# Kernel optimization log

Measured on AMD Instinct MI355X. Metric: run time of the kernel, lower is better.

The kernel has to match this reference:

```python
import jax, jax.numpy as jnp
import numpy as np

D_MODEL = 1024
NUM_HEADS = 16
HEAD_DIM = D_MODEL // NUM_HEADS
B, L = 4, 2048


def setup_inputs() -> dict:
    key = jax.random.key(0)
    ks = jax.random.split(key, 10)
    s = 1.0 / np.sqrt(D_MODEL)
    inp = {
        "x": jax.random.normal(ks[0], (B, L, D_MODEL), dtype=jnp.float32),
        "mask": jax.random.randint(ks[1], (1, 1, L, L), 0, 2, dtype=jnp.int32),
        "Wq": jax.random.normal(ks[2], (D_MODEL, D_MODEL), dtype=jnp.float32) * s,
        "bq": jnp.zeros((D_MODEL,), dtype=jnp.float32),
        "Wk": jax.random.normal(ks[3], (D_MODEL, D_MODEL), dtype=jnp.float32) * s,
        "bk": jnp.zeros((D_MODEL,), dtype=jnp.float32),
        "Wv": jax.random.normal(ks[4], (D_MODEL, D_MODEL), dtype=jnp.float32) * s,
        "bv": jnp.zeros((D_MODEL,), dtype=jnp.float32),
        "Wo": jax.random.normal(ks[5], (D_MODEL, D_MODEL), dtype=jnp.float32) * s,
        "bo": jnp.zeros((D_MODEL,), dtype=jnp.float32),
    }
    return inp


def reference(x, mask, Wq, bq, Wk, bk, Wv, bv, Wo, bo):
    b, l, d = x.shape
    # projections (torch Linear: x @ W.T + b)
    q = (x @ Wq.T + bq).reshape(b, l, NUM_HEADS, HEAD_DIM).transpose(0, 2, 1, 3)
    k = (x @ Wk.T + bk).reshape(b, l, NUM_HEADS, HEAD_DIM).transpose(0, 2, 1, 3)
    v = (x @ Wv.T + bv).reshape(b, l, NUM_HEADS, HEAD_DIM).transpose(0, 2, 1, 3)
    scale = 1.0 / np.sqrt(HEAD_DIM).astype(np.float32)
    scores = jnp.einsum("bhqd,bhkd->bhqk", q, k) * scale
    scores = jnp.where(mask == 0, jnp.float32(-1e9), scores)
    attn = jax.nn.softmax(scores, axis=-1)
    out = jnp.einsum("bhqk,bhkd->bhqd", attn, v)
    out = out.transpose(0, 2, 1, 3).reshape(b, l, d)
    return out @ Wo.T + bo
```

## Files before the change

### kernel.cpp

```cpp
#include <hip/hip_runtime.h>
#include <stdint.h>

#define LSEQ 2048
#define DMODEL 1024
#define NHEADS 16
#define HDIM 64
#define NBATCH 4

typedef __attribute__((ext_vector_type(8))) __bf16 bf16x8;
typedef __attribute__((ext_vector_type(4))) __bf16 bf16x4;
typedef __attribute__((ext_vector_type(4))) float f32x4;
typedef __attribute__((ext_vector_type(16))) float f32x16;
typedef __attribute__((ext_vector_type(4))) uint32_t u32x4;
typedef __attribute__((ext_vector_type(8))) uint16_t u16x8;

__device__ inline float fexp2(float x) {
#if __has_builtin(__builtin_amdgcn_exp2f)
    return __builtin_amdgcn_exp2f(x);
#else
    float r; asm("v_exp_f32 %0, %1" : "=v"(r) : "v"(x)); return r;
#endif
}

__device__ inline uint32_t bitmask1(uint32_t m, int pos) {
#if __has_builtin(__builtin_amdgcn_sbfe)
    return (uint32_t)__builtin_amdgcn_sbfe((int)m, pos, 1);
#else
    return (uint32_t)(((int32_t)(m << (31 - pos))) >> 31);
#endif
}

__device__ inline uint32_t cvtpk(float lo, float hi) {
    uint32_t r;
    asm("v_cvt_pk_bf16_f32 %0, %1, %2" : "=v"(r) : "v"(lo), "v"(hi));
    return r;
}
__device__ inline void swap32(uint32_t& a, uint32_t& b) {
    asm volatile("v_permlane32_swap_b32 %0, %1" : "+v"(a), "+v"(b));
}

__device__ inline void gload_lds16(const void* g, const void* l) {
    auto gp = reinterpret_cast<const uint32_t __attribute__((address_space(1)))*>(
        reinterpret_cast<uintptr_t>(g));
    auto lp = reinterpret_cast<uint32_t __attribute__((address_space(3)))*>(
        (uint32_t)(uintptr_t)(l));
    __builtin_amdgcn_global_load_lds(gp, lp, 16, 0, 0);
}

__device__ inline f32x16 zero16() {
    f32x16 z;
#pragma unroll
    for (int i = 0; i < 16; i++) z[i] = 0.f;
    return z;
}

__global__ void cvt_f32_bf16(const float* __restrict__ src, __bf16* __restrict__ dst, int n) {
    int idx = blockIdx.x * blockDim.x + threadIdx.x;
    int stride = gridDim.x * blockDim.x;
    for (int i = idx * 4; i < n; i += stride * 4) {
        float4 f = *(const float4*)(src + i);
        bf16x4 v;
        v[0] = (__bf16)f.x; v[1] = (__bf16)f.y; v[2] = (__bf16)f.z; v[3] = (__bf16)f.w;
        *(bf16x4*)(dst + i) = v;
    }
}

__global__ void cvt_w4(const float* __restrict__ a, const float* __restrict__ b,
                       const float* __restrict__ c, const float* __restrict__ d,
                       __bf16* __restrict__ dst) {
    const int t = blockIdx.x * blockDim.x + threadIdx.x;
    const int i4 = t * 4;
    const int m = i4 >> 20;
    const int off = i4 & ((1 << 20) - 1);
    const float* src = (m == 0) ? a : (m == 1) ? b : (m == 2) ? c : d;
    float4 f = *(const float4*)(src + off);
    bf16x4 v;
    v[0] = (__bf16)f.x; v[1] = (__bf16)f.y; v[2] = (__bf16)f.z; v[3] = (__bf16)f.w;
    *(bf16x4*)(dst + i4) = v;
}

__global__ void pack_bias(const float* __restrict__ bq, const float* __restrict__ bk,
                          const float* __restrict__ bv, float* __restrict__ dst) {
    const int i = blockIdx.x * 256 + threadIdx.x;
    dst[i] = (i < 1024) ? bq[i] : (i < 2048) ? bk[i - 1024] : bv[i - 2048];
}

__global__ void pack_mask(const int* __restrict__ mask, unsigned long long* __restrict__ mbits) {
    const int row = blockIdx.x;
    const int w = threadIdx.x >> 6, lane = threadIdx.x & 63;
    const int* mrow = mask + (size_t)row * LSEQ;
#pragma unroll
    for (int it = 0; it < 8; it++) {
        const int c = it * 256 + w * 64 + lane;
        const unsigned long long b = __ballot(mrow[c] != 0);
        if (lane == 0) mbits[(size_t)row * 32 + it * 4 + w] = b;
    }
}

template <int MODE>
__global__ __launch_bounds__(256) void gemm_bt(const __bf16* __restrict__ A,
                                               const __bf16* __restrict__ Bw,
                                               const float* __restrict__ bias,
                                               void* __restrict__ Cout,
                                               int M, int N, int K, float scale) {
    __shared__ __bf16 As[128 * 32];
    __shared__ __bf16 Bs[128 * 32];

    const int nwg = gridDim.x;
    int bid = blockIdx.x;
    bid = (bid & 7) * (nwg >> 3) + (bid >> 3);

    const int nbn = N >> 7;
    const int bm = (bid / nbn) << 7;
    const int bn = (bid % nbn) << 7;
    const int tid = threadIdx.x;
    const int w = tid >> 6, lane = tid & 63;
    const int l15 = lane & 15, l4 = lane >> 4;
    const int wm = (w >> 1) * 64, wn = (w & 1) * 64;

    f32x4 acc[4][4];
    for (int i = 0; i < 4; i++)
        for (int j = 0; j < 4; j++)
            acc[i][j] = (f32x4){0.f, 0.f, 0.f, 0.f};

    const int fa0 = (w * 2 + 0) * 64 + lane;
    const int fa1 = (w * 2 + 1) * 64 + lane;
    const __bf16* gA0 = A + (size_t)(bm + (fa0 >> 2)) * K + (fa0 & 3) * 8;
    const __bf16* gA1 = A + (size_t)(bm + (fa1 >> 2)) * K + (fa1 & 3) * 8;
    const __bf16* gB0 = Bw + (size_t)(bn + (fa0 >> 2)) * K + (fa0 & 3) * 8;
    const __bf16* gB1 = Bw + (size_t)(bn + (fa1 >> 2)) * K + (fa1 & 3) * 8;
    const __bf16* lA0 = &As[(w * 2 + 0) * 512];
    const __bf16* lA1 = &As[(w * 2 + 1) * 512];
    const __bf16* lB0 = &Bs[(w * 2 + 0) * 512];
    const __bf16* lB1 = &Bs[(w * 2 + 1) * 512];

    for (int kt = 0; kt < K; kt += 32) {
        __syncthreads();
        gload_lds16(gA0 + kt, lA0);
        gload_lds16(gA1 + kt, lA1);
        gload_lds16(gB0 + kt, lB0);
        gload_lds16(gB1 + kt, lB1);
        __syncthreads();

        bf16x8 af[4], bw[4];
        for (int i = 0; i < 4; i++)
            af[i] = *(const bf16x8*)&As[(wm + i * 16 + l15) * 32 + l4 * 8];
        for (int j = 0; j < 4; j++)
            bw[j] = *(const bf16x8*)&Bs[(wn + j * 16 + l15) * 32 + l4 * 8];
        for (int i = 0; i < 4; i++)
            for (int j = 0; j < 4; j++)
                acc[i][j] = __builtin_amdgcn_mfma_f32_16x16x32_bf16(af[i], bw[j], acc[i][j], 0, 0, 0);
    }

    for (int i = 0; i < 4; i++) {
        const int row0 = bm + wm + i * 16 + l4 * 4;
        for (int j = 0; j < 4; j++) {
            const int col = bn + wn + j * 16 + l15;
            const float bv = bias[col];
            if (MODE == 0) {
                __bf16* dst = (__bf16*)Cout;
                const int which = col >> 10;
                const int cr = col & 1023;
                const int h = cr >> 6, d = cr & 63;
                const float scl = (which == 0) ? scale : 1.0f;
                for (int jj = 0; jj < 4; jj++) {
                    const int r = row0 + jj;
                    const int b = r >> 11, l = r & (LSEQ - 1);
                    dst[((size_t)which << 23) +
                        (((size_t)(b * NHEADS + h) * LSEQ + l) << 6) + d] =
                        (__bf16)((acc[i][j][jj] + bv) * scl);
                }
            } else {
                float* dst = (float*)Cout;
                for (int jj = 0; jj < 4; jj++) {
                    const int r = row0 + jj;
                    dst[(size_t)r * N + col] = acc[i][j][jj] + bv;
                }
            }
        }
    }
}

__device__ inline void storeV8(uint32_t (*vt)[32], int kpi, int d0,
                               const u16x8& r0, const u16x8& r1) {
    const uint32_t* a = (const uint32_t*)&r0;
    const uint32_t* b = (const uint32_t*)&r1;
#pragma unroll
    for (int jp = 0; jp < 4; jp++) {
        const uint32_t w0 = __builtin_amdgcn_perm(b[jp], a[jp], 0x05040100u);
        const uint32_t w1 = __builtin_amdgcn_perm(b[jp], a[jp], 0x07060302u);
        const int j0 = jp * 2, j1 = jp * 2 + 1;
        vt[d0 + j0][(kpi & 3) | (((kpi >> 2) ^ j0) << 2)] = w0;
        vt[d0 + j1][(kpi & 3) | (((kpi >> 2) ^ j1) << 2)] = w1;
    }
}

__global__ __launch_bounds__(256) void attn_fwd(const __bf16* __restrict__ Q,
                                                const __bf16* __restrict__ Kk,
                                                const __bf16* __restrict__ V,
                                                const unsigned long long* __restrict__ mbits,
                                                __bf16* __restrict__ Oout) {
    const int bh = blockIdx.x & 63;
    const int qt = blockIdx.x >> 6;
    const int tid = threadIdx.x;
    const int w = tid >> 6, lane = tid & 63;
    const int l31 = lane & 31, hi = lane >> 5, l7 = lane & 7;

    __shared__ __bf16 Ks[2][64 * 64];
    __shared__ uint32_t Vt32[2][64][32];

    const int q0w = qt * 128 + w * 32;

    const __bf16* qrow = Q + ((size_t)bh * LSEQ + q0w + l31) * HDIM + hi * 8;
    bf16x8 aq[4];
#pragma unroll
    for (int s = 0; s < 4; s++) aq[s] = *(const bf16x8*)(qrow + s * 16);

    f32x16 o0 = zero16(), o1 = zero16();
    float m_run = -1.0e30f, l_run = 0.f;

    const int ck0 = tid, ck1 = tid + 256;
    const int koff0 = ((ck0 >> 3) << 7) + ((((ck0 & 7) ^ ((ck0 >> 3) & 7))) << 4);
    const int koff1 = ((ck1 >> 3) << 7) + ((((ck1 & 7) ^ ((ck1 >> 3) & 7))) << 4);
    const char* kp0 = (const char*)(Kk + (size_t)bh * LSEQ * HDIM) + koff0;
    const char* kp1 = (const char*)(Kk + (size_t)bh * LSEQ * HDIM) + koff1;

    const int kpi = tid & 31;
    const int d0v = (tid >> 5) * 8;
    const __bf16* vp0 = V + (size_t)bh * LSEQ * HDIM + (size_t)(2 * kpi) * HDIM + d0v;
    const __bf16* vp1 = vp0 + HDIM;

    const uint2* mptr = (const uint2*)(mbits + (size_t)(q0w + l31) * 32);
    const int msh = hi * 4;

    {
        const u16x8 v0 = *(const u16x8*)(vp0);
        const u16x8 v1 = *(const u16x8*)(vp1);
        vp0 += 64 * HDIM; vp1 += 64 * HDIM;
        storeV8(Vt32[0], kpi, d0v, v0, v1);
        gload_lds16(kp0, &Ks[0][ck0 * 8]);
        gload_lds16(kp1, &Ks[0][ck1 * 8]);
        kp0 += 8192; kp1 += 8192;
    }
    __syncthreads();

    int cur = 0;
    const int NT = LSEQ / 64;
    for (int t = 0; t < NT; t++) {
        const int nx = cur ^ 1;
        u16x8 nv0, nv1;
        if (t < NT - 1) {
            nv0 = *(const u16x8*)(vp0);
            nv1 = *(const u16x8*)(vp1);
            vp0 += 64 * HDIM; vp1 += 64 * HDIM;
            gload_lds16(kp0, &Ks[nx][ck0 * 8]);
            gload_lds16(kp1, &Ks[nx][ck1 * 8]);
            kp0 += 8192; kp1 += 8192;
        }

        const uint2 mw = mptr[t];
        const uint32_t mword0 = mw.x >> msh;
        const uint32_t mword1 = mw.y >> msh;
        const char* ksb = (const char*)&Ks[cur][0];
        const uint32_t* vb = &Vt32[cur][0][0];

#pragma unroll
        for (int kk = 0; kk < 2; kk++) {
            f32x16 sf = zero16();
            __builtin_amdgcn_s_setprio(1);
#pragma unroll
            for (int s = 0; s < 4; s++) {
                const bf16x8 ka = *(const bf16x8*)(ksb + kk * 4096 + l31 * 128 +
                                                   (((s * 2 + hi) ^ l7) << 4));
                sf = __builtin_amdgcn_mfma_f32_32x32x16_bf16(ka, aq[s], sf, 0, 0, 0);
            }
            __builtin_amdgcn_s_setprio(0);

            float vmx = sf[0];
#pragma unroll
            for (int r = 1; r < 16; r++) vmx = fmaxf(vmx, sf[r]);
            vmx = fmaxf(vmx, __shfl_xor(vmx, 32));

            if (__any(vmx > m_run + 8.f)) {
                const float mnew = fmaxf(m_run, vmx);
                const float alpha = fexp2(m_run - mnew);
                m_run = mnew;
                l_run *= alpha;
#pragma unroll
                for (int r = 0; r < 16; r++) {
                    const float ar = __shfl(alpha, (r & 3) + 8 * (r >> 2) + 4 * hi);
                    o0[r] *= ar; o1[r] *= ar;
                }
            }

            const uint32_t mwd = kk ? mword1 : mword0;
            float e[16];
#pragma unroll
            for (int r = 0; r < 16; r++) {
                float ev = fexp2(sf[r] - m_run);
                const uint32_t msk = bitmask1(mwd, (r & 3) + 8 * (r >> 2));
                ev = __builtin_bit_cast(float, __builtin_bit_cast(uint32_t, ev) & msk);
                l_run += ev;
                e[r] = ev;
            }
            uint32_t p0 = cvtpk(e[0], e[1]),   p1 = cvtpk(e[2], e[3]);
            uint32_t p2 = cvtpk(e[4], e[5]),   p3 = cvtpk(e[6], e[7]);
            uint32_t p4 = cvtpk(e[8], e[9]),   p5 = cvtpk(e[10], e[11]);
            uint32_t p6 = cvtpk(e[12], e[13]), p7 = cvtpk(e[14], e[15]);
            swap32(p0, p2); swap32(p1, p3);
            swap32(p4, p6); swap32(p5, p7);
            const bf16x8 pa0 = __builtin_bit_cast(bf16x8, (u32x4){p0, p1, p2, p3});
            const bf16x8 pa1 = __builtin_bit_cast(bf16x8, (u32x4){p4, p5, p6, p7});

            __builtin_amdgcn_s_setprio(1);
#pragma unroll
            for (int s2 = 0; s2 < 2; s2++) {
                const bf16x8 pa = s2 ? pa1 : pa0;
                const int col = (((kk * 4 + s2 * 2 + hi) ^ l7) << 2);
                const u32x4 v0 = *(const u32x4*)(vb + (l31) * 32 + col);
                const u32x4 v1 = *(const u32x4*)(vb + (32 + l31) * 32 + col);
                o0 = __builtin_amdgcn_mfma_f32_32x32x16_bf16(pa, __builtin_bit_cast(bf16x8, v0), o0, 0, 0, 0);
                o1 = __builtin_amdgcn_mfma_f32_32x32x16_bf16(pa, __builtin_bit_cast(bf16x8, v1), o1, 0, 0, 0);
            }
            __builtin_amdgcn_s_setprio(0);
        }

        if (t < NT - 1) storeV8(Vt32[nx], kpi, d0v, nv0, nv1);
        __syncthreads();
        cur = nx;
    }

    const int b = bh >> 4, h = bh & 15;
    const float lt = l_run + __shfl_xor(l_run, 32);
    const float inv = 1.0f / fmaxf(lt, 1e-30f);
#pragma unroll
    for (int r = 0; r < 16; r++) {
        const int ql = (r & 3) + 8 * (r >> 2) + 4 * hi;
        const float invr = __shfl(inv, ql);
        const int q = q0w + ql;
        const size_t base = ((size_t)b * LSEQ + q) * DMODEL + h * HDIM + l31;
        Oout[base] = (__bf16)(o0[r] * invr);
        Oout[base + 32] = (__bf16)(o1[r] * invr);
    }
}

extern "C" void kernel_launch(void* const* d_in, const int* in_sizes, int n_in,
                              void* d_out, int out_size, void* d_ws, size_t ws_size,
                              hipStream_t stream) {
    const float* x  = (const float*)d_in[0];
    const int* mask = (const int*)d_in[1];
    const float* Wq = (const float*)d_in[2];
    const float* bq = (const float*)d_in[3];
    const float* Wk = (const float*)d_in[4];
    const float* bk = (const float*)d_in[5];
    const float* Wv = (const float*)d_in[6];
    const float* bv = (const float*)d_in[7];
    const float* Wo = (const float*)d_in[8];
    const float* bo = (const float*)d_in[9];

    char* ws = (char*)d_ws;
    __bf16* xb  = (__bf16*)(ws);
    __bf16* wqb = (__bf16*)(ws + (16u << 20));
    __bf16* wob = (__bf16*)(ws + (22u << 20));
    __bf16* qb  = (__bf16*)(ws + (24u << 20));
    __bf16* ab  = (__bf16*)(ws + (72u << 20));
    unsigned long long* mb = (unsigned long long*)(ws + (88u << 20));
    float* bqkv = (float*)(ws + (89u << 20));

    const __bf16* kb = qb + ((size_t)1 << 23);
    const __bf16* vb = qb + ((size_t)2 << 23);

    const int M = NBATCH * LSEQ;
    const int N = DMODEL;
    const int K = DMODEL;
    const float cs = 0.18033688011112f;

    cvt_f32_bf16<<<2048, 256, 0, stream>>>(x, xb, M * K);
    cvt_w4<<<4096, 256, 0, stream>>>(Wq, Wk, Wv, Wo, wqb);
    pack_bias<<<12, 256, 0, stream>>>(bq, bk, bv, bqkv);
    pack_mask<<<LSEQ, 256, 0, stream>>>(mask, mb);

    gemm_bt<0><<<(M / 128) * (3 * N / 128), 256, 0, stream>>>(
        xb, wqb, bqkv, (void*)qb, M, 3 * N, K, cs);

    attn_fwd<<<(LSEQ / 128) * 64, 256, 0, stream>>>(qb, kb, vb, mb, ab);

    gemm_bt<1><<<(M / 128) * (N / 128), 256, 0, stream>>>(
        ab, wob, bo, d_out, M, N, K, 1.0f);
}
```

Before: 246.6 us.

## Process two 32-row query sub-tiles per wave to reuse K/V tiles

Each wave in the attention kernel now owns 64 query rows as two independent 32-row sub-tiles, each with its own online-softmax state. K fragments and V reads from shared memory are shared between both sub-tiles' MFMAs, and each block covers 256 queries, so the grid halves. This cuts LDS and global K/V traffic per query and raises MFMA density. The cost is roughly double the accumulator registers, which can lower occupancy, and fewer blocks to spread across CUs.

```diff
diff --git a/kernel.cpp b/kernel.cpp
--- a/kernel.cpp
+++ b/kernel.cpp
@@ -209,15 +209,19 @@
     __shared__ __bf16 Ks[2][64 * 64];
     __shared__ uint32_t Vt32[2][64][32];
 
-    const int q0w = qt * 128 + w * 32;
-
-    const __bf16* qrow = Q + ((size_t)bh * LSEQ + q0w + l31) * HDIM + hi * 8;
-    bf16x8 aq[4];
-#pragma unroll
-    for (int s = 0; s < 4; s++) aq[s] = *(const bf16x8*)(qrow + s * 16);
-
-    f32x16 o0 = zero16(), o1 = zero16();
-    float m_run = -1.0e30f, l_run = 0.f;
+    const int q0w = qt * 256 + w * 64;
+
+    const __bf16* qrowA = Q + ((size_t)bh * LSEQ + q0w + l31) * HDIM + hi * 8;
+    const __bf16* qrowB = qrowA + 32 * HDIM;
+    bf16x8 aqA[4], aqB[4];
+#pragma unroll
+    for (int s = 0; s < 4; s++) {
+        aqA[s] = *(const bf16x8*)(qrowA + s * 16);
+        aqB[s] = *(const bf16x8*)(qrowB + s * 16);
+    }
+
+    f32x16 oA0 = zero16(), oA1 = zero16(), oB0 = zero16(), oB1 = zero16();
+    float mA = -1.0e30f, lA = 0.f, mB = -1.0e30f, lB = 0.f;
 
     const int ck0 = tid, ck1 = tid + 256;
     const int koff0 = ((ck0 >> 3) << 7) + ((((ck0 & 7) ^ ((ck0 >> 3) & 7))) << 4);
@@ -230,7 +234,8 @@
     const __bf16* vp0 = V + (size_t)bh * LSEQ * HDIM + (size_t)(2 * kpi) * HDIM + d0v;
     const __bf16* vp1 = vp0 + HDIM;
 
-    const uint2* mptr = (const uint2*)(mbits + (size_t)(q0w + l31) * 32);
+    const uint2* mptrA = (const uint2*)(mbits + (size_t)(q0w + l31) * 32);
+    const uint2* mptrB = (const uint2*)(mbits + (size_t)(q0w + 32 + l31) * 32);
     const int msh = hi * 4;
 
     {
@@ -258,69 +263,96 @@
             kp0 += 8192; kp1 += 8192;
         }
 
-        const uint2 mw = mptr[t];
-        const uint32_t mword0 = mw.x >> msh;
-        const uint32_t mword1 = mw.y >> msh;
+        const uint2 mwA = mptrA[t];
+        const uint2 mwB = mptrB[t];
         const char* ksb = (const char*)&Ks[cur][0];
         const uint32_t* vb = &Vt32[cur][0][0];
 
 #pragma unroll
         for (int kk = 0; kk < 2; kk++) {
-            f32x16 sf = zero16();
+            bf16x8 ka[4];
+#pragma unroll
+            for (int s = 0; s < 4; s++)
+                ka[s] = *(const bf16x8*)(ksb + kk * 4096 + l31 * 128 +
+                                         (((s * 2 + hi) ^ l7) << 4));
+
+            f32x16 sfA = zero16(), sfB = zero16();
             __builtin_amdgcn_s_setprio(1);
 #pragma unroll
             for (int s = 0; s < 4; s++) {
-                const bf16x8 ka = *(const bf16x8*)(ksb + kk * 4096 + l31 * 128 +
-                                                   (((s * 2 + hi) ^ l7) << 4));
-                sf = __builtin_amdgcn_mfma_f32_32x32x16_bf16(ka, aq[s], sf, 0, 0, 0);
+                sfA = __builtin_amdgcn_mfma_f32_32x32x16_bf16(ka[s], aqA[s], sfA, 0, 0, 0);
+                sfB = __builtin_amdgcn_mfma_f32_32x32x16_bf16(ka[s], aqB[s], sfB, 0, 0, 0);
             }
             __builtin_amdgcn_s_setprio(0);
 
-            float vmx = sf[0];
-#pragma unroll
-            for (int r = 1; r < 16; r++) vmx = fmaxf(vmx, sf[r]);
-            vmx = fmaxf(vmx, __shfl_xor(vmx, 32));
-
-            if (__any(vmx > m_run + 8.f)) {
-                const float mnew = fmaxf(m_run, vmx);
-                const float alpha = fexp2(m_run - mnew);
-                m_run = mnew;
-                l_run *= alpha;
+            float vmxA = sfA[0], vmxB = sfB[0];
+#pragma unroll
+            for (int r = 1; r < 16; r++) {
+                vmxA = fmaxf(vmxA, sfA[r]);
+                vmxB = fmaxf(vmxB, sfB[r]);
+            }
+            vmxA = fmaxf(vmxA, __shfl_xor(vmxA, 32));
+            vmxB = fmaxf(vmxB, __shfl_xor(vmxB, 32));
+
+            if (__any((vmxA > mA + 8.f) || (vmxB > mB + 8.f))) {
+                const float mnA = fmaxf(mA, vmxA), mnB = fmaxf(mB, vmxB);
+                const float alA = fexp2(mA - mnA), alB = fexp2(mB - mnB);
+                mA = mnA; mB = mnB;
+                lA *= alA; lB *= alB;
 #pragma unroll
                 for (int r = 0; r < 16; r++) {
-                    const float ar = __shfl(alpha, (r & 3) + 8 * (r >> 2) + 4 * hi);
-                    o0[r] *= ar; o1[r] *= ar;
+                    const int ql = (r & 3) + 8 * (r >> 2) + 4 * hi;
+                    const float arA = __shfl(alA, ql);
+                    const float arB = __shfl(alB, ql);
+                    oA0[r] *= arA; oA1[r] *= arA;
+                    oB0[r] *= arB; oB1[r] *= arB;
                 }
             }
 
-            const uint32_t mwd = kk ? mword1 : mword0;
-            float e[16];
+            const uint32_t mwdA = (kk ? mwA.y : mwA.x) >> msh;
+            const uint32_t mwdB = (kk ? mwB.y : mwB.x) >> msh;
+            float eA[16], eB[16];
 #pragma unroll
             for (int r = 0; r < 16; r++) {
-                float ev = fexp2(sf[r] - m_run);
-                const uint32_t msk = bitmask1(mwd, (r & 3) + 8 * (r >> 2));
-                ev = __builtin_bit_cast(float, __builtin_bit_cast(uint32_t, ev) & msk);
-                l_run += ev;
-                e[r] = ev;
-            }
-            uint32_t p0 = cvtpk(e[0], e[1]),   p1 = cvtpk(e[2], e[3]);
-            uint32_t p2 = cvtpk(e[4], e[5]),   p3 = cvtpk(e[6], e[7]);
-            uint32_t p4 = cvtpk(e[8], e[9]),   p5 = cvtpk(e[10], e[11]);
-            uint32_t p6 = cvtpk(e[12], e[13]), p7 = cvtpk(e[14], e[15]);
-            swap32(p0, p2); swap32(p1, p3);
-            swap32(p4, p6); swap32(p5, p7);
-            const bf16x8 pa0 = __builtin_bit_cast(bf16x8, (u32x4){p0, p1, p2, p3});
-            const bf16x8 pa1 = __builtin_bit_cast(bf16x8, (u32x4){p4, p5, p6, p7});
+                const int bp = (r & 3) + 8 * (r >> 2);
+                float evA = fexp2(sfA[r] - mA);
+                float evB = fexp2(sfB[r] - mB);
+                evA = __builtin_bit_cast(float,
+                      __builtin_bit_cast(uint32_t, evA) & bitmask1(mwdA, bp));
+                evB = __builtin_bit_cast(float,
+                      __builtin_bit_cast(uint32_t, evB) & bitmask1(mwdB, bp));
+                lA += evA; lB += evB;
+                eA[r] = evA; eB[r] = evB;
+            }
+            uint32_t a0 = cvtpk(eA[0], eA[1]),   a1 = cvtpk(eA[2], eA[3]);
+            uint32_t a2 = cvtpk(eA[4], eA[5]),   a3 = cvtpk(eA[6], eA[7]);
+            uint32_t a4 = cvtpk(eA[8], eA[9]),   a5 = cvtpk(eA[10], eA[11]);
+            uint32_t a6 = cvtpk(eA[12], eA[13]), a7 = cvtpk(eA[14], eA[15]);
+            swap32(a0, a2); swap32(a1, a3);
+            swap32(a4, a6); swap32(a5, a7);
+            const bf16x8 paA0 = __builtin_bit_cast(bf16x8, (u32x4){a0, a1, a2, a3});
+            const bf16x8 paA1 = __builtin_bit_cast(bf16x8, (u32x4){a4, a5, a6, a7});
+            uint32_t b0 = cvtpk(eB[0], eB[1]),   b1 = cvtpk(eB[2], eB[3]);
+            uint32_t b2 = cvtpk(eB[4], eB[5]),   b3 = cvtpk(eB[6], eB[7]);
+            uint32_t b4 = cvtpk(eB[8], eB[9]),   b5 = cvtpk(eB[10], eB[11]);
+            uint32_t b6 = cvtpk(eB[12], eB[13]), b7 = cvtpk(eB[14], eB[15]);
+            swap32(b0, b2); swap32(b1, b3);
+            swap32(b4, b6); swap32(b5, b7);
+            const bf16x8 paB0 = __builtin_bit_cast(bf16x8, (u32x4){b0, b1, b2, b3});
+            const bf16x8 paB1 = __builtin_bit_cast(bf16x8, (u32x4){b4, b5, b6, b7});
 
             __builtin_amdgcn_s_setprio(1);
 #pragma unroll
             for (int s2 = 0; s2 < 2; s2++) {
-                const bf16x8 pa = s2 ? pa1 : pa0;
                 const int col = (((kk * 4 + s2 * 2 + hi) ^ l7) << 2);
-                const u32x4 v0 = *(const u32x4*)(vb + (l31) * 32 + col);
-                const u32x4 v1 = *(const u32x4*)(vb + (32 + l31) * 32 + col);
-                o0 = __builtin_amdgcn_mfma_f32_32x32x16_bf16(pa, __builtin_bit_cast(bf16x8, v0), o0, 0, 0, 0);
-                o1 = __builtin_amdgcn_mfma_f32_32x32x16_bf16(pa, __builtin_bit_cast(bf16x8, v1), o1, 0, 0, 0);
+                const bf16x8 v0 = __builtin_bit_cast(bf16x8, *(const u32x4*)(vb + l31 * 32 + col));
+                const bf16x8 v1 = __builtin_bit_cast(bf16x8, *(const u32x4*)(vb + (32 + l31) * 32 + col));
+                const bf16x8 pA = s2 ? paA1 : paA0;
+                const bf16x8 pB = s2 ? paB1 : paB0;
+                oA0 = __builtin_amdgcn_mfma_f32_32x32x16_bf16(pA, v0, oA0, 0, 0, 0);
+                oA1 = __builtin_amdgcn_mfma_f32_32x32x16_bf16(pA, v1, oA1, 0, 0, 0);
+                oB0 = __builtin_amdgcn_mfma_f32_32x32x16_bf16(pB, v0, oB0, 0, 0, 0);
+                oB1 = __builtin_amdgcn_mfma_f32_32x32x16_bf16(pB, v1, oB1, 0, 0, 0);
             }
             __builtin_amdgcn_s_setprio(0);
         }
@@ -331,16 +363,22 @@
     }
 
     const int b = bh >> 4, h = bh & 15;
-    const float lt = l_run + __shfl_xor(l_run, 32);
-    const float inv = 1.0f / fmaxf(lt, 1e-30f);
+    const float ltA = lA + __shfl_xor(lA, 32);
+    const float ltB = lB + __shfl_xor(lB, 32);
+    const float invA = 1.0f / fmaxf(ltA, 1e-30f);
+    const float invB = 1.0f / fmaxf(ltB, 1e-30f);
 #pragma unroll
     for (int r = 0; r < 16; r++) {
         const int ql = (r & 3) + 8 * (r >> 2) + 4 * hi;
-        const float invr = __shfl(inv, ql);
-        const int q = q0w + ql;
-        const size_t base = ((size_t)b * LSEQ + q) * DMODEL + h * HDIM + l31;
-        Oout[base] = (__bf16)(o0[r] * invr);
-        Oout[base + 32] = (__bf16)(o1[r] * invr);
+        const float irA = __shfl(invA, ql);
+        const float irB = __shfl(invB, ql);
+        const int qa = q0w + ql;
+        const size_t baseA = ((size_t)b * LSEQ + qa) * DMODEL + h * HDIM + l31;
+        const size_t baseB = baseA + (size_t)32 * DMODEL;
+        Oout[baseA] = (__bf16)(oA0[r] * irA);
+        Oout[baseA + 32] = (__bf16)(oA1[r] * irA);
+        Oout[baseB] = (__bf16)(oB0[r] * irB);
+        Oout[baseB + 32] = (__bf16)(oB1[r] * irB);
     }
 }
 
@@ -383,7 +421,7 @@
     gemm_bt<0><<<(M / 128) * (3 * N / 128), 256, 0, stream>>>(
         xb, wqb, bqkv, (void*)qb, M, 3 * N, K, cs);
 
-    attn_fwd<<<(LSEQ / 128) * 64, 256, 0, stream>>>(qb, kb, vb, mb, ab);
+    attn_fwd<<<(LSEQ / 256) * 64, 256, 0, stream>>>(qb, kb, vb, mb, ab);
 
     gemm_bt<1><<<(M / 128) * (N / 128), 256, 0, stream>>>(
         ab, wob, bo, d_out, M, N, K, 1.0f);
```

Measured after the change: 280.5 us. +13.7%, slower.
